# Performance work log

Measured on AMD Instinct MI355X. Metric: run time of the kernel, lower is better.

Reference implementation:

```python
import math
import jax, jax.numpy as jnp
import numpy as np

B, N, DIM = 2, 4096, 768
H, DK, DV = 8, 64, 64


def setup_inputs() -> dict:
    key = jax.random.key(0)
    ks = jax.random.split(key, 6)
    s = 0.02
    return {
        "x": jax.random.normal(ks[0], (B, N, DIM), dtype=jnp.float32),
        "Wq": jax.random.normal(ks[1], (DIM, H * DK), dtype=jnp.float32) * s,
        "Wk": jax.random.normal(ks[2], (DIM, H * DK), dtype=jnp.float32) * s,
        "Wv": jax.random.normal(ks[3], (DIM, H * DV), dtype=jnp.float32) * s,
        "Wo": jax.random.normal(ks[4], (H * DV, DIM), dtype=jnp.float32) * s,
        "bo": jax.random.normal(ks[5], (DIM,), dtype=jnp.float32) * s,
    }


def reference(x, Wq, Wk, Wv, Wo, bo):
    b, n, _ = x.shape
    # project and split heads: [B, H, N, d]
    q = (x @ Wq).reshape(b, n, H, DK).transpose(0, 2, 1, 3)
    k = (x @ Wk).reshape(b, n, H, DK).transpose(0, 2, 1, 3)
    v = (x @ Wv).reshape(b, n, H, DV).transpose(0, 2, 1, 3)
    scale = 1.0 / math.sqrt(DK)
    scores = jnp.einsum("bhnd,bhmd->bhnm", q, k) * scale  # [B,H,N,N]
    attn = jax.nn.softmax(scores, axis=-1)
    out = jnp.einsum("bhnm,bhmd->bhnd", attn, v)  # [B,H,N,DV]
    out = out.transpose(0, 2, 1, 3).reshape(b, n, H * DV)
    return out @ Wo + bo
```

## Files before the change

kernel.cpp:

```cpp
#include <hip/hip_runtime.h>
#include <hip/hip_bf16.h>

#define B_   2
#define N_   4096
#define DIM_ 768
#define H_   8
#define MROWS_ 8192

typedef __bf16 bf16x8 __attribute__((ext_vector_type(8)));
typedef __bf16 bf16x4 __attribute__((ext_vector_type(4)));
typedef float  f32x4  __attribute__((ext_vector_type(4)));

static __device__ __forceinline__ f32x4 mfma16(bf16x8 a, bf16x8 b, f32x4 c) {
    return __builtin_amdgcn_mfma_f32_16x16x32_bf16(a, b, c, 0, 0, 0);
}

#define GLDS16(g, l) \
    __builtin_amdgcn_global_load_lds((const __attribute__((address_space(1))) void*)(g), \
                                     (__attribute__((address_space(3))) void*)(l), 16, 0, 0)

__global__ void cvt_x_kernel(const float* __restrict__ x, __bf16* __restrict__ xb, int n4) {
    int i = blockIdx.x * blockDim.x + threadIdx.x;
    if (i >= n4) return;
    float4 f = reinterpret_cast<const float4*>(x)[i];
    bf16x4 o;
    o[0] = (__bf16)f.x; o[1] = (__bf16)f.y; o[2] = (__bf16)f.z; o[3] = (__bf16)f.w;
    reinterpret_cast<bf16x4*>(xb)[i] = o;
}

__global__ __launch_bounds__(256) void transpose_w_kernel(const float* __restrict__ Wq,
                                                          const float* __restrict__ Wk,
                                                          const float* __restrict__ Wv,
                                                          const float* __restrict__ Wo,
                                                          __bf16* __restrict__ wt,
                                                          __bf16* __restrict__ wot) {
    __shared__ float tile[64][65];
    const int bix = blockIdx.x;
    const float* src;
    int src_ld, rbase, cbase, dst_ld, drow, dcol;
    __bf16* dst;
    if (bix < 288) {
        int m = bix / 96, t = bix - m * 96;
        int tr = t >> 3, tc = t & 7;
        src = (m == 0) ? Wq : ((m == 1) ? Wk : Wv);
        src_ld = 512; rbase = tr * 64; cbase = tc * 64;
        dst = wt; dst_ld = 768; drow = m * 512 + tc * 64; dcol = tr * 64;
    } else {
        int t = bix - 288;
        int tr = t / 12, tc = t - tr * 12;
        src = Wo; src_ld = 768; rbase = tr * 64; cbase = tc * 64;
        dst = wot; dst_ld = 512; drow = tc * 64; dcol = tr * 64;
    }
#pragma unroll
    for (int kk = 0; kk < 4; ++kk) {
        int idx = threadIdx.x + kk * 256;
        int r = idx >> 4, c = (idx & 15) << 2;
        float4 f = *reinterpret_cast<const float4*>(&src[(size_t)(rbase + r) * src_ld + cbase + c]);
        tile[r][c] = f.x; tile[r][c + 1] = f.y; tile[r][c + 2] = f.z; tile[r][c + 3] = f.w;
    }
    __syncthreads();
#pragma unroll
    for (int kk = 0; kk < 4; ++kk) {
        int idx = threadIdx.x + kk * 256;
        int r = idx >> 4, c = (idx & 15) << 2;
        bf16x4 ov;
        ov[0] = (__bf16)tile[c][r];     ov[1] = (__bf16)tile[c + 1][r];
        ov[2] = (__bf16)tile[c + 2][r]; ov[3] = (__bf16)tile[c + 3][r];
        *reinterpret_cast<bf16x4*>(&dst[(size_t)(drow + r) * dst_ld + dcol + c]) = ov;
    }
}

template<int KSTEPS>
__device__ __forceinline__ void gemm_tile_main(const __bf16* __restrict__ A, const int lda,
                                               const int arow0,
                                               const __bf16* __restrict__ Bt, const int ldb,
                                               const int bcol0,
                                               __bf16* __restrict__ abuf,
                                               __bf16* __restrict__ bbuf,
                                               f32x4 (&acc)[4][4]) {
    const int lane = threadIdx.x & 63, wave = threadIdx.x >> 6;
    const int lr = lane & 15, lg = lane >> 4;
    const int wr = wave >> 1, wc = wave & 1;

    const int cid0 = wave * 128 + lane;
    const int cid1 = cid0 + 64;
    const __bf16* sA0 = A  + (size_t)(arow0 + (cid0 >> 2)) * lda + (cid0 & 3) * 8;
    const __bf16* sA1 = A  + (size_t)(arow0 + (cid1 >> 2)) * lda + (cid1 & 3) * 8;
    const __bf16* sB0 = Bt + (size_t)(bcol0 + (cid0 >> 2)) * ldb + (cid0 & 3) * 8;
    const __bf16* sB1 = Bt + (size_t)(bcol0 + (cid1 >> 2)) * ldb + (cid1 & 3) * 8;

    auto stage = [&](int buf, int ks) {
        __bf16* da = abuf + buf * 4096 + wave * 1024;
        __bf16* db = bbuf + buf * 4096 + wave * 1024;
        GLDS16(sA0 + ks * 32, da);
        GLDS16(sA1 + ks * 32, da + 512);
        GLDS16(sB0 + ks * 32, db);
        GLDS16(sB1 + ks * 32, db + 512);
    };

    stage(0, 0);
    asm volatile("s_waitcnt vmcnt(0)" ::: "memory");
    __syncthreads();

    const int ar_off = (wr * 64 + lr) * 32 + lg * 8;
    const int br_off = (wc * 64 + lr) * 32 + lg * 8;

    int buf = 0;
    for (int ks = 0; ks < KSTEPS; ++ks) {
        if (ks + 1 < KSTEPS) stage(buf ^ 1, ks + 1);
        const __bf16* ab = abuf + buf * 4096 + ar_off;
        const __bf16* bb = bbuf + buf * 4096 + br_off;
        bf16x8 af[4], bfr[4];
#pragma unroll
        for (int m = 0; m < 4; ++m) af[m] = *reinterpret_cast<const bf16x8*>(ab + m * 512);
#pragma unroll
        for (int n = 0; n < 4; ++n) bfr[n] = *reinterpret_cast<const bf16x8*>(bb + n * 512);
#pragma unroll
        for (int m = 0; m < 4; ++m)
#pragma unroll
            for (int n = 0; n < 4; ++n)
                acc[m][n] = mfma16(af[m], bfr[n], acc[m][n]);
        asm volatile("s_waitcnt vmcnt(0)" ::: "memory");
        __syncthreads();
        buf ^= 1;
    }
}

__global__ __launch_bounds__(256) void qkv_gemm_kernel(const __bf16* __restrict__ xb,
                                                       const __bf16* __restrict__ wt,
                                                       __bf16* __restrict__ q,
                                                       __bf16* __restrict__ k,
                                                       __bf16* __restrict__ vt) {
    __shared__ __align__(16) __bf16 abuf[2 * 4096];
    __shared__ __align__(16) __bf16 bbuf[2 * 4096];

    const int bid = blockIdx.x;
    const int vb = (bid & 7) * 96 + (bid >> 3);
    const int by = vb % 12, bx = vb / 12;

    f32x4 acc[4][4] = {};
    gemm_tile_main<24>(xb, 768, bx * 128, wt, 768, by * 128, abuf, bbuf, acc);

    const int lane = threadIdx.x & 63, wave = threadIdx.x >> 6;
    const int lr = lane & 15, lg = lane >> 4;
    const int wr = wave >> 1, wc = wave & 1;
    const int bi = (bx * 128) >> 12;
    const int nbase = (bx * 128) & 4095;

    const float QSCALE = 0.125f * 1.44269504089f;

#pragma unroll
    for (int n = 0; n < 4; ++n) {
        const int col0 = by * 128 + wc * 64 + n * 16;
        const int mtx = col0 >> 9;
        const int h   = (col0 >> 6) & 7;
        const int d0  = (col0 & 63) + lr;
        const size_t hb = (size_t)(bi * 8 + h);
#pragma unroll
        for (int m = 0; m < 4; ++m) {
            const int nn = nbase + wr * 64 + m * 16 + lg * 4;
            if (mtx == 0) {
#pragma unroll
                for (int r = 0; r < 4; ++r)
                    q[(hb * 4096 + nn + r) * 64 + d0] = (__bf16)(acc[m][n][r] * QSCALE);
            } else if (mtx == 1) {
#pragma unroll
                for (int r = 0; r < 4; ++r)
                    k[(hb * 4096 + nn + r) * 64 + d0] = (__bf16)acc[m][n][r];
            } else {
                bf16x4 ov;
#pragma unroll
                for (int r = 0; r < 4; ++r) ov[r] = (__bf16)acc[m][n][r];
                *reinterpret_cast<bf16x4*>(&vt[(hb * 64 + d0) * 4096 + nn]) = ov;
            }
        }
    }
}

__global__ __launch_bounds__(512, 4) void attn_kernel(const __bf16* __restrict__ q,
                                                      const __bf16* __restrict__ k,
                                                      const __bf16* __restrict__ vt,
                                                      __bf16* __restrict__ o) {
    const int lane = threadIdx.x & 63, wave = threadIdx.x >> 6;
    const int lr = lane & 15, lg = lane >> 4;
    const int qg = wave >> 1, kh = wave & 1;

    const int bid  = blockIdx.x;
    const int vbid = (bid & 7) * 64 + (bid >> 3);
    const int qtile = vbid & 31;
    const int bh    = vbid >> 5;
    const int qbase = qtile * 128 + qg * 32;

    const __bf16* Qh = q  + (size_t)bh * N_ * 64;
    const __bf16* Kh = k  + (size_t)bh * N_ * 64;
    const __bf16* Vh = vt + (size_t)bh * 64 * N_;

    __shared__ __align__(16) char smem[49152];
    __bf16* kb0 = (__bf16*)smem;
    __bf16* vb0 = (__bf16*)(smem + 24576);

    const int l8 = lane >> 3, l7 = lane & 7;
    const int swz8 = (l7 ^ l8) * 8;

    int ksrc[2];
#pragma unroll
    for (int c = 0; c < 2; ++c) {
        int i = wave * 16 + c * 8 + l8;
        int sig = ((i >> 4) & 1) * 32 + ((i >> 2) & 3) * 8 + ((i >> 5) & 1) * 4 + (i & 3);
        ksrc[c] = sig * 64 + swz8;
    }

    auto kslot = [&](int s) { return kb0 + s * 4096; };
    auto vslot = [&](int s) { return vb0 + s * 4096; };

    auto stageK = [&](int slot, int jt) {
        if (wave < 4) {
            const __bf16* srcb = Kh + (size_t)jt * 4096;
            __bf16* dst = kslot(slot) + wave * 1024;
            GLDS16(srcb + ksrc[0], dst);
            GLDS16(srcb + ksrc[1], dst + 512);
        }
    };
    auto stageV = [&](int slot, int jt) {
        if (wave >= 4) {
            const int w2 = wave - 4;
            const __bf16* src = Vh + (size_t)(w2 * 16 + l8) * 4096 + jt * 64 + swz8;
            __bf16* dst = vslot(slot) + w2 * 1024;
            GLDS16(src, dst);
            GLDS16(src + (size_t)8 * 4096, dst + 512);
        }
    };

    bf16x8 qf[2][2];
#pragma unroll
    for (int f = 0; f < 2; ++f)
#pragma unroll
        for (int kc = 0; kc < 2; ++kc)
            qf[f][kc] = *reinterpret_cast<const bf16x8*>(
                Qh + (size_t)(qbase + f * 16 + lr) * 64 + kc * 32 + lg * 8);

    f32x4 acc[2][4] = {};
    f32x4 accl[2] = {};
    bf16x8 vones;
#pragma unroll
    for (int t = 0; t < 8; ++t) vones[t] = (__bf16)1.0f;

    f32x4 s[2][2];
    bf16x8 pk[2];

    auto QK = [&](const __bf16* kb_) {
        const char* kb = (const char*)kb_;
        __builtin_amdgcn_s_setprio(1);
#pragma unroll
        for (int kc = 0; kc < 2; ++kc) {
#pragma unroll
            for (int c2 = 0; c2 < 2; ++c2) {
                const int row = (kh + 2 * c2) * 16 + lr;
                bf16x8 bk = *reinterpret_cast<const bf16x8*>(
                    kb + row * 128 + (((kc * 4 + lg) ^ (lr & 7)) << 4));
#pragma unroll
                for (int f = 0; f < 2; ++f) {
                    if (kc == 0) s[f][c2] = mfma16(bk, qf[f][0], {});
                    else         s[f][c2] = mfma16(bk, qf[f][1], s[f][c2]);
                }
            }
        }
        __builtin_amdgcn_s_setprio(0);
    };
    auto EXP = [&]() {
#pragma unroll
        for (int f = 0; f < 2; ++f) {
#pragma unroll
            for (int t = 0; t < 8; ++t)
                pk[f][t] = (__bf16)__builtin_amdgcn_exp2f(s[f][t >> 2][t & 3]);
            accl[f] = mfma16(pk[f], vones, accl[f]);
        }
    };
    auto PV = [&](const __bf16* vb_) {
        const char* vb = (const char*)vb_;
        __builtin_amdgcn_s_setprio(1);
#pragma unroll
        for (int cbv = 0; cbv < 4; ++cbv) {
            const int row = cbv * 16 + lr;
            bf16x8 bv = *reinterpret_cast<const bf16x8*>(
                vb + row * 128 + (((kh * 4 + lg) ^ (lr & 7)) << 4));
#pragma unroll
            for (int f = 0; f < 2; ++f)
                acc[f][cbv] = mfma16(pk[f], bv, acc[f][cbv]);
        }
        __builtin_amdgcn_s_setprio(0);
    };

    auto ITER = [&](int kr, int kw, int ktile, int vr, int vw, int vtile) {
        stageK(kw, ktile);
        stageV(vw, vtile);
        QK(kslot(kr));
        PV(vslot(vr));
        EXP();
        asm volatile("s_waitcnt vmcnt(2)" ::: "memory");
        __builtin_amdgcn_s_barrier();
    };

    stageK(0, 0); stageK(1, 1); stageV(0, 0);
    asm volatile("s_waitcnt vmcnt(0)" ::: "memory");
    __builtin_amdgcn_s_barrier();

    stageK(2, 2); stageV(1, 1);
    QK(kslot(0));
    EXP();
    asm volatile("s_waitcnt vmcnt(2)" ::: "memory");
    __builtin_amdgcn_s_barrier();

    for (int t = 0; t < 20; ++t) {
        const int a = 3 * t + 1;
        ITER(1, 0, a + 2, 0, 2, a + 1);
        ITER(2, 1, a + 3, 1, 0, a + 2);
        ITER(0, 2, a + 4, 2, 1, a + 3);
    }
    ITER(1, 0, 63, 0, 2, 62);

    stageV(0, 63);
    QK(kslot(2));
    PV(vslot(1));
    EXP();
    asm volatile("s_waitcnt vmcnt(0)" ::: "memory");
    __builtin_amdgcn_s_barrier();

    QK(kslot(0));
    PV(vslot(2));
    EXP();
    asm volatile("s_waitcnt vmcnt(0)" ::: "memory");
    __builtin_amdgcn_s_barrier();

    PV(vslot(0));
    __syncthreads();

    char* exa = smem + qg * 4096;
    char* exl = smem + 16384 + qg * 2048;
    if (kh == 1) {
#pragma unroll
        for (int f = 0; f < 2; ++f) {
#pragma unroll
            for (int cbv = 0; cbv < 4; ++cbv) {
                bf16x4 p4;
#pragma unroll
                for (int r = 0; r < 4; ++r) p4[r] = (__bf16)acc[f][cbv][r];
                *reinterpret_cast<bf16x4*>(exa + lane * 64 + (f * 4 + cbv) * 8) = p4;
            }
            *reinterpret_cast<f32x4*>(exl + lane * 32 + f * 16) = accl[f];
        }
    }
    __syncthreads();

    if (kh == 0) {
        const int b = bh >> 3, h = bh & 7;
#pragma unroll
        for (int f = 0; f < 2; ++f) {
            f32x4 lp = *reinterpret_cast<const f32x4*>(exl + lane * 32 + f * 16);
            f32x4 inv;
#pragma unroll
            for (int r = 0; r < 4; ++r) inv[r] = 1.f / (accl[f][r] + lp[r]);
#pragma unroll
            for (int cbv = 0; cbv < 4; ++cbv) {
                bf16x4 ap = *reinterpret_cast<const bf16x4*>(exa + lane * 64 + (f * 4 + cbv) * 8);
#pragma unroll
                for (int r = 0; r < 4; ++r) {
                    const int row = b * N_ + qbase + f * 16 + lg * 4 + r;
                    o[(size_t)row * 512 + h * 64 + cbv * 16 + lr] =
                        (__bf16)((acc[f][cbv][r] + (float)ap[r]) * inv[r]);
                }
            }
        }
    }
}

__global__ __launch_bounds__(256) void out_gemm_kernel(const __bf16* __restrict__ ob,
                                                       const __bf16* __restrict__ wot,
                                                       const float* __restrict__ bo,
                                                       float* __restrict__ out) {
    __shared__ __align__(16) __bf16 abuf[2 * 4096];
    __shared__ __align__(16) __bf16 bbuf[2 * 4096];

    const int bid = blockIdx.x;
    const int vb = (bid & 7) * 48 + (bid >> 3);
    const int by = vb % 6, bx = vb / 6;

    f32x4 acc[4][4] = {};
    gemm_tile_main<16>(ob, 512, bx * 128, wot, 512, by * 128, abuf, bbuf, acc);

    const int lane = threadIdx.x & 63, wave = threadIdx.x >> 6;
    const int lr = lane & 15, lg = lane >> 4;
    const int wr = wave >> 1, wc = wave & 1;

#pragma unroll
    for (int n = 0; n < 4; ++n) {
        const int col = by * 128 + wc * 64 + n * 16 + lr;
        const float bias = bo[col];
#pragma unroll
        for (int m = 0; m < 4; ++m) {
            const int row0 = bx * 128 + wr * 64 + m * 16 + lg * 4;
#pragma unroll
            for (int r = 0; r < 4; ++r)
                out[(size_t)(row0 + r) * 768 + col] = acc[m][n][r] + bias;
        }
    }
}

extern "C" void kernel_launch(void* const* d_in, const int* in_sizes, int n_in,
                              void* d_out, int out_size, void* d_ws, size_t ws_size,
                              hipStream_t stream) {
    const float* x  = (const float*)d_in[0];
    const float* Wq = (const float*)d_in[1];
    const float* Wk = (const float*)d_in[2];
    const float* Wv = (const float*)d_in[3];
    const float* Wo = (const float*)d_in[4];
    const float* bo = (const float*)d_in[5];
    float* out = (float*)d_out;

    char* ws = (char*)d_ws;
    __bf16* xb  = (__bf16*)(ws);
    __bf16* wt  = (__bf16*)(ws + 12582912);
    __bf16* wot = (__bf16*)(ws + 12582912 + 2359296);
    char*   p0  = ws + 12582912 + 2359296 + 786432;
    __bf16* qw  = (__bf16*)(p0);
    __bf16* kw  = (__bf16*)(p0 + 8388608);
    __bf16* vtw = (__bf16*)(p0 + 2 * (size_t)8388608);
    __bf16* obf = (__bf16*)(p0 + 3 * (size_t)8388608);

    cvt_x_kernel<<<6144, 256, 0, stream>>>(x, xb, MROWS_ * DIM_ / 4);
    transpose_w_kernel<<<384, 256, 0, stream>>>(Wq, Wk, Wv, Wo, wt, wot);
    qkv_gemm_kernel<<<768, 256, 0, stream>>>(xb, wt, qw, kw, vtw);
    attn_kernel<<<512, 512, 0, stream>>>(qw, kw, vtw, obf);
    out_gemm_kernel<<<384, 256, 0, stream>>>(obf, wot, bo, out);
}
```

Before: 122.9 us.

## Store Q/K/V in FP8 and run attention matmuls with FP8 MFMA

The QKV projection epilogue now writes Q, K and V^T as FP8 e4m3 bytes instead of bf16. The attention kernel loads them with halved LDS staging (one 16-byte global-to-LDS load per lane, new swizzle) and uses the 16x16x32 fp8 MFMA for QK^T, PV and the row-sum. The exponentiated probabilities are also packed to FP8. The aim is to cut global and LDS traffic and shared-memory footprint, at the cost of substantially lower numerical precision in scores, probabilities and values.

```diff
diff --git a/kernel.cpp b/kernel.cpp
--- a/kernel.cpp
+++ b/kernel.cpp
@@ -13,6 +13,9 @@
 
 static __device__ __forceinline__ f32x4 mfma16(bf16x8 a, bf16x8 b, f32x4 c) {
     return __builtin_amdgcn_mfma_f32_16x16x32_bf16(a, b, c, 0, 0, 0);
+}
+static __device__ __forceinline__ f32x4 mfma_fp8(long long a, long long b, f32x4 c) {
+    return __builtin_amdgcn_mfma_f32_16x16x32_fp8_fp8(a, b, c, 0, 0, 0);
 }
 
 #define GLDS16(g, l) \
@@ -128,9 +131,9 @@
 
 __global__ __launch_bounds__(256) void qkv_gemm_kernel(const __bf16* __restrict__ xb,
                                                        const __bf16* __restrict__ wt,
-                                                       __bf16* __restrict__ q,
-                                                       __bf16* __restrict__ k,
-                                                       __bf16* __restrict__ vt) {
+                                                       unsigned char* __restrict__ q,
+                                                       unsigned char* __restrict__ k,
+                                                       unsigned char* __restrict__ vt) {
     __shared__ __align__(16) __bf16 abuf[2 * 4096];
     __shared__ __align__(16) __bf16 bbuf[2 * 4096];
 
@@ -161,25 +164,31 @@
             const int nn = nbase + wr * 64 + m * 16 + lg * 4;
             if (mtx == 0) {
 #pragma unroll
-                for (int r = 0; r < 4; ++r)
-                    q[(hb * 4096 + nn + r) * 64 + d0] = (__bf16)(acc[m][n][r] * QSCALE);
+                for (int r = 0; r < 4; ++r) {
+                    float v = acc[m][n][r] * QSCALE;
+                    int p = __builtin_amdgcn_cvt_pk_fp8_f32(v, v, 0, 0);
+                    q[((hb * 4096 + nn + r) << 6) + d0] = (unsigned char)(p & 0xFF);
+                }
             } else if (mtx == 1) {
 #pragma unroll
-                for (int r = 0; r < 4; ++r)
-                    k[(hb * 4096 + nn + r) * 64 + d0] = (__bf16)acc[m][n][r];
+                for (int r = 0; r < 4; ++r) {
+                    float v = acc[m][n][r];
+                    int p = __builtin_amdgcn_cvt_pk_fp8_f32(v, v, 0, 0);
+                    k[((hb * 4096 + nn + r) << 6) + d0] = (unsigned char)(p & 0xFF);
+                }
             } else {
-                bf16x4 ov;
-#pragma unroll
-                for (int r = 0; r < 4; ++r) ov[r] = (__bf16)acc[m][n][r];
-                *reinterpret_cast<bf16x4*>(&vt[(hb * 64 + d0) * 4096 + nn]) = ov;
+                int vv = 0;
+                vv = __builtin_amdgcn_cvt_pk_fp8_f32(acc[m][n][0], acc[m][n][1], vv, 0);
+                vv = __builtin_amdgcn_cvt_pk_fp8_f32(acc[m][n][2], acc[m][n][3], vv, 1);
+                *reinterpret_cast<int*>(&vt[(hb * 64 + d0) * 4096 + nn]) = vv;
             }
         }
     }
 }
 
-__global__ __launch_bounds__(512, 4) void attn_kernel(const __bf16* __restrict__ q,
-                                                      const __bf16* __restrict__ k,
-                                                      const __bf16* __restrict__ vt,
+__global__ __launch_bounds__(512, 4) void attn_kernel(const unsigned char* __restrict__ q,
+                                                      const unsigned char* __restrict__ k,
+                                                      const unsigned char* __restrict__ vt,
                                                       __bf16* __restrict__ o) {
     const int lane = threadIdx.x & 63, wave = threadIdx.x >> 6;
     const int lr = lane & 15, lg = lane >> 4;
@@ -191,77 +200,78 @@
     const int bh    = vbid >> 5;
     const int qbase = qtile * 128 + qg * 32;
 
-    const __bf16* Qh = q  + (size_t)bh * N_ * 64;
-    const __bf16* Kh = k  + (size_t)bh * N_ * 64;
-    const __bf16* Vh = vt + (size_t)bh * 64 * N_;
-
-    __shared__ __align__(16) char smem[49152];
-    __bf16* kb0 = (__bf16*)smem;
-    __bf16* vb0 = (__bf16*)(smem + 24576);
-
-    const int l8 = lane >> 3, l7 = lane & 7;
-    const int swz8 = (l7 ^ l8) * 8;
-
-    int ksrc[2];
-#pragma unroll
-    for (int c = 0; c < 2; ++c) {
-        int i = wave * 16 + c * 8 + l8;
-        int sig = ((i >> 4) & 1) * 32 + ((i >> 2) & 3) * 8 + ((i >> 5) & 1) * 4 + (i & 3);
-        ksrc[c] = sig * 64 + swz8;
-    }
-
-    auto kslot = [&](int s) { return kb0 + s * 4096; };
-    auto vslot = [&](int s) { return vb0 + s * 4096; };
+    const unsigned char* Qh = q  + (size_t)bh * N_ * 64;
+    const unsigned char* Kh = k  + (size_t)bh * N_ * 64;
+    const unsigned char* Vh = vt + (size_t)bh * 64 * N_;
+
+    __shared__ __align__(16) char smem[24576];
+    char* kb0 = smem;
+    char* vb0 = smem + 12288;
+
+    int ksrcOff = 0;
+    size_t vsrcOff = 0;
+    if (wave < 4) {
+        int ci = wave * 64 + lane;
+        int r = ci >> 2, c = ci & 3;
+        int sig = ((r >> 4) & 1) * 32 + ((r >> 2) & 3) * 8 + ((r >> 5) & 1) * 4 + (r & 3);
+        ksrcOff = sig * 64 + ((c ^ ((r & 3) ^ ((r >> 2) & 3))) << 4);
+    } else {
+        int ci = (wave - 4) * 64 + lane;
+        int r = ci >> 2, c = ci & 3;
+        vsrcOff = (size_t)r * 4096 + ((c ^ ((r & 3) ^ ((r >> 2) & 3))) << 4);
+    }
 
     auto stageK = [&](int slot, int jt) {
-        if (wave < 4) {
-            const __bf16* srcb = Kh + (size_t)jt * 4096;
-            __bf16* dst = kslot(slot) + wave * 1024;
-            GLDS16(srcb + ksrc[0], dst);
-            GLDS16(srcb + ksrc[1], dst + 512);
-        }
+        if (wave < 4)
+            GLDS16(Kh + (size_t)jt * 4096 + ksrcOff, kb0 + slot * 4096 + wave * 1024);
     };
     auto stageV = [&](int slot, int jt) {
-        if (wave >= 4) {
-            const int w2 = wave - 4;
-            const __bf16* src = Vh + (size_t)(w2 * 16 + l8) * 4096 + jt * 64 + swz8;
-            __bf16* dst = vslot(slot) + w2 * 1024;
-            GLDS16(src, dst);
-            GLDS16(src + (size_t)8 * 4096, dst + 512);
-        }
-    };
-
-    bf16x8 qf[2][2];
+        if (wave >= 4)
+            GLDS16(Vh + vsrcOff + jt * 64, vb0 + slot * 4096 + (wave - 4) * 1024);
+    };
+
+    int kaddr[2][2], vaddr[4];
+#pragma unroll
+    for (int kc = 0; kc < 2; ++kc)
+#pragma unroll
+        for (int c2 = 0; c2 < 2; ++c2) {
+            int row = (kh + 2 * c2) * 16 + lr;
+            int x = (row & 3) ^ ((row >> 2) & 3);
+            kaddr[kc][c2] = row * 64 + (((kc * 2 + (lg >> 1)) ^ x) << 4) + ((lg & 1) << 3);
+        }
+#pragma unroll
+    for (int cbv = 0; cbv < 4; ++cbv) {
+        int row = cbv * 16 + lr;
+        int x = (row & 3) ^ ((row >> 2) & 3);
+        vaddr[cbv] = row * 64 + (((kh * 2 + (lg >> 1)) ^ x) << 4) + ((lg & 1) << 3);
+    }
+
+    long long qf[2][2];
 #pragma unroll
     for (int f = 0; f < 2; ++f)
 #pragma unroll
         for (int kc = 0; kc < 2; ++kc)
-            qf[f][kc] = *reinterpret_cast<const bf16x8*>(
+            qf[f][kc] = *reinterpret_cast<const long long*>(
                 Qh + (size_t)(qbase + f * 16 + lr) * 64 + kc * 32 + lg * 8);
 
     f32x4 acc[2][4] = {};
     f32x4 accl[2] = {};
-    bf16x8 vones;
-#pragma unroll
-    for (int t = 0; t < 8; ++t) vones[t] = (__bf16)1.0f;
+    const long long ONES8 = 0x3838383838383838LL;
 
     f32x4 s[2][2];
-    bf16x8 pk[2];
-
-    auto QK = [&](const __bf16* kb_) {
-        const char* kb = (const char*)kb_;
+    long long pk[2];
+
+    auto QK = [&](const char* kb) {
         __builtin_amdgcn_s_setprio(1);
 #pragma unroll
         for (int kc = 0; kc < 2; ++kc) {
 #pragma unroll
             for (int c2 = 0; c2 < 2; ++c2) {
-                const int row = (kh + 2 * c2) * 16 + lr;
-                bf16x8 bk = *reinterpret_cast<const bf16x8*>(
-                    kb + row * 128 + (((kc * 4 + lg) ^ (lr & 7)) << 4));
+                long long bk = *reinterpret_cast<const long long*>(kb + kaddr[kc][c2]);
 #pragma unroll
                 for (int f = 0; f < 2; ++f) {
-                    if (kc == 0) s[f][c2] = mfma16(bk, qf[f][0], {});
-                    else         s[f][c2] = mfma16(bk, qf[f][1], s[f][c2]);
+                    if (kc == 0) s[f][c2] = mfma_fp8(bk, qf[f][0], {});
+                    else         s[f][c2] = mfma_fp8(bk, qf[f][1], s[f][c2]);
                 }
             }
         }
@@ -270,34 +280,45 @@
     auto EXP = [&]() {
 #pragma unroll
         for (int f = 0; f < 2; ++f) {
-#pragma unroll
-            for (int t = 0; t < 8; ++t)
-                pk[f][t] = (__bf16)__builtin_amdgcn_exp2f(s[f][t >> 2][t & 3]);
-            accl[f] = mfma16(pk[f], vones, accl[f]);
-        }
-    };
-    auto PV = [&](const __bf16* vb_) {
-        const char* vb = (const char*)vb_;
+            float p0 = __builtin_amdgcn_exp2f(s[f][0][0]);
+            float p1 = __builtin_amdgcn_exp2f(s[f][0][1]);
+            float p2 = __builtin_amdgcn_exp2f(s[f][0][2]);
+            float p3 = __builtin_amdgcn_exp2f(s[f][0][3]);
+            float p4 = __builtin_amdgcn_exp2f(s[f][1][0]);
+            float p5 = __builtin_amdgcn_exp2f(s[f][1][1]);
+            float p6 = __builtin_amdgcn_exp2f(s[f][1][2]);
+            float p7 = __builtin_amdgcn_exp2f(s[f][1][3]);
+            int lo = 0, hi = 0;
+            lo = __builtin_amdgcn_cvt_pk_fp8_f32(p0, p1, lo, 0);
+            lo = __builtin_amdgcn_cvt_pk_fp8_f32(p2, p3, lo, 1);
+            hi = __builtin_amdgcn_cvt_pk_fp8_f32(p4, p5, hi, 0);
+            hi = __builtin_amdgcn_cvt_pk_fp8_f32(p6, p7, hi, 1);
+            pk[f] = (long long)(unsigned int)lo | ((long long)hi << 32);
+            accl[f] = mfma_fp8(pk[f], ONES8, accl[f]);
+        }
+    };
+    auto PV = [&](const char* vb) {
         __builtin_amdgcn_s_setprio(1);
 #pragma unroll
         for (int cbv = 0; cbv < 4; ++cbv) {
-            const int row = cbv * 16 + lr;
-            bf16x8 bv = *reinterpret_cast<const bf16x8*>(
-                vb + row * 128 + (((kh * 4 + lg) ^ (lr & 7)) << 4));
+            long long bv = *reinterpret_cast<const long long*>(vb + vaddr[cbv]);
 #pragma unroll
             for (int f = 0; f < 2; ++f)
-                acc[f][cbv] = mfma16(pk[f], bv, acc[f][cbv]);
+                acc[f][cbv] = mfma_fp8(pk[f], bv, acc[f][cbv]);
         }
         __builtin_amdgcn_s_setprio(0);
     };
+
+    auto kslotp = [&](int sl) { return (const char*)(kb0 + sl * 4096); };
+    auto vslotp = [&](int sl) { return (const char*)(vb0 + sl * 4096); };
 
     auto ITER = [&](int kr, int kw, int ktile, int vr, int vw, int vtile) {
         stageK(kw, ktile);
         stageV(vw, vtile);
-        QK(kslot(kr));
-        PV(vslot(vr));
+        QK(kslotp(kr));
+        PV(vslotp(vr));
         EXP();
-        asm volatile("s_waitcnt vmcnt(2)" ::: "memory");
+        asm volatile("s_waitcnt vmcnt(1)" ::: "memory");
         __builtin_amdgcn_s_barrier();
     };
 
@@ -306,9 +327,9 @@
     __builtin_amdgcn_s_barrier();
 
     stageK(2, 2); stageV(1, 1);
-    QK(kslot(0));
+    QK(kslotp(0));
     EXP();
-    asm volatile("s_waitcnt vmcnt(2)" ::: "memory");
+    asm volatile("s_waitcnt vmcnt(1)" ::: "memory");
     __builtin_amdgcn_s_barrier();
 
     for (int t = 0; t < 20; ++t) {
@@ -320,19 +341,19 @@
     ITER(1, 0, 63, 0, 2, 62);
 
     stageV(0, 63);
-    QK(kslot(2));
-    PV(vslot(1));
+    QK(kslotp(2));
+    PV(vslotp(1));
     EXP();
     asm volatile("s_waitcnt vmcnt(0)" ::: "memory");
     __builtin_amdgcn_s_barrier();
 
-    QK(kslot(0));
-    PV(vslot(2));
+    QK(kslotp(0));
+    PV(vslotp(2));
     EXP();
     asm volatile("s_waitcnt vmcnt(0)" ::: "memory");
     __builtin_amdgcn_s_barrier();
 
-    PV(vslot(0));
+    PV(vslotp(0));
     __syncthreads();
 
     char* exa = smem + qg * 4096;
@@ -422,10 +443,10 @@
     __bf16* wt  = (__bf16*)(ws + 12582912);
     __bf16* wot = (__bf16*)(ws + 12582912 + 2359296);
     char*   p0  = ws + 12582912 + 2359296 + 786432;
-    __bf16* qw  = (__bf16*)(p0);
-    __bf16* kw  = (__bf16*)(p0 + 8388608);
-    __bf16* vtw = (__bf16*)(p0 + 2 * (size_t)8388608);
-    __bf16* obf = (__bf16*)(p0 + 3 * (size_t)8388608);
+    unsigned char* qw  = (unsigned char*)(p0);
+    unsigned char* kw  = (unsigned char*)(p0 + 4194304);
+    unsigned char* vtw = (unsigned char*)(p0 + 2 * 4194304);
+    __bf16* obf = (__bf16*)(p0 + 3 * (size_t)4194304);
 
     cvt_x_kernel<<<6144, 256, 0, stream>>>(x, xb, MROWS_ * DIM_ / 4);
     transpose_w_kernel<<<384, 256, 0, stream>>>(Wq, Wk, Wv, Wo, wt, wot);
```

Measured after the change: 116.1 us. 1.06x faster.
